# Kernel tuning notes

Hardware: AMD Instinct MI355X
Metric: run time of the kernel (lower is better)

## Reference

```python
import jax, jax.numpy as jnp
import numpy as np

N, D, C = 8192, 10000, 1000


def setup_inputs() -> dict:
    key = jax.random.key(0)
    k1, k2 = jax.random.split(key)
    # binary {0,1} hypervectors, stored as float32 for efficient GEMM-form Hamming distance
    samples = jax.random.randint(k1, (N, D), 0, 2).astype(jnp.float32)
    classes_hv = jax.random.randint(k2, (C, D), 0, 2).astype(jnp.float32)
    return {"samples": samples, "classes_hv": classes_hv}


def reference(samples, classes_hv):
    # Original: response[i] = sum_d xor(samples[:, d], classes_hv[i, d])  (Hamming distance)
    # For binary a,b: xor(a,b) = a + b - 2*a*b, so the full [N, C] distance matrix is
    # dist = row_sum(samples)[:, None] + row_sum(hv)[None, :] - 2 * samples @ hv.T
    # This replaces the per-class XOR+reduce loop with one GEMM (same math).
    s_sum = jnp.sum(samples, axis=-1)          # [N]
    c_sum = jnp.sum(classes_hv, axis=-1)       # [C]
    cross = jnp.einsum('nd,cd->nc', samples, classes_hv)  # [N, C]
    return s_sum[:, None] + c_sum[None, :] - 2.0 * cross  # [N, C] Hamming distances
```

## Files before the change

### kernel.cpp

```cpp
#include <hip/hip_runtime.h>
#include <stdint.h>

#define N_ROWS 8192
#define C_CLS  1000
#define D_DIM  10000
#define W64P   160
#define W32P   (W64P * 2)
#define BKW    16
#define NCHUNK 20

typedef int v4i  __attribute__((ext_vector_type(4)));
typedef int v16i __attribute__((ext_vector_type(16)));

__global__ __launch_bounds__(256) void pack_kernel(
    const float* __restrict__ samples, const float* __restrict__ classes,
    unsigned long long* __restrict__ pA, unsigned long long* __restrict__ pB,
    uint32_t* __restrict__ rsA, uint32_t* __restrict__ rsB)
{
    int gwave = (blockIdx.x * 256 + threadIdx.x) >> 6;
    int lane  = threadIdx.x & 63;
    if (gwave >= N_ROWS + C_CLS) return;

    const float* src;
    unsigned long long* dst;
    uint32_t* rsw;
    if (gwave < N_ROWS) {
        src = samples + (size_t)gwave * D_DIM;
        dst = pA + (size_t)gwave * W64P;
        rsw = rsA + gwave;
    } else {
        int r = gwave - N_ROWS;
        src = classes + (size_t)r * D_DIM;
        dst = pB + (size_t)r * W64P;
        rsw = rsB + r;
    }

    uint32_t rs = 0;
    #pragma unroll 4
    for (int w = 0; w < 40; ++w) {
        int idx = w * 256 + lane * 4;
        float4 v = make_float4(0.f, 0.f, 0.f, 0.f);
        if (idx < D_DIM) v = *(const float4*)(src + idx);
        unsigned long long m0 = __ballot(v.x > 0.5f);
        unsigned long long m1 = __ballot(v.y > 0.5f);
        unsigned long long m2 = __ballot(v.z > 0.5f);
        unsigned long long m3 = __ballot(v.w > 0.5f);
        rs += (uint32_t)(__popcll(m0) + __popcll(m1) + __popcll(m2) + __popcll(m3));
        if (lane == 0) {
            uint4 p0, p1;
            p0.x = (uint32_t)m0; p0.y = (uint32_t)(m0 >> 32);
            p0.z = (uint32_t)m1; p0.w = (uint32_t)(m1 >> 32);
            p1.x = (uint32_t)m2; p1.y = (uint32_t)(m2 >> 32);
            p1.z = (uint32_t)m3; p1.w = (uint32_t)(m3 >> 32);
            *(uint4*)(dst + (size_t)w * 4)     = p0;
            *(uint4*)(dst + (size_t)w * 4 + 2) = p1;
        }
    }
    if (lane == 0) *rsw = rs;
}

__global__ __launch_bounds__(256) void hd_kernel(
    const uint32_t* __restrict__ pA, const uint32_t* __restrict__ pB,
    const uint32_t* __restrict__ rsA, const uint32_t* __restrict__ rsB,
    float* __restrict__ out)
{
    __shared__ uint32_t AsT[2][(BKW / 2) * 256];
    __shared__ uint32_t BsT[2][(BKW / 2) * 256];

    const int tid  = threadIdx.x;
    const int row0 = blockIdx.x * 128;
    const int col0 = blockIdx.y * 128;

    const int w    = tid >> 6;
    const int lane = tid & 63;
    const int wy   = w >> 1;
    const int wx   = w & 1;
    const int ln   = lane & 31;
    const int h4   = (lane >> 5) * 4;
    const int pb   = 2 * w;

    const int srow = tid >> 1;
    const int sq2  = (tid & 1) * 2;
    const uint32_t* gAs = pA + (size_t)(row0 + srow) * W32P + sq2 * 4;
    int gc = col0 + srow; if (gc >= C_CLS) gc = C_CLS - 1;
    const uint32_t* gBs = pB + (size_t)gc * W32P + sq2 * 4;

    uint4 av[2], bv[2];

#define LOADR(ch) do {                                             \
    av[0] = *(const uint4*)(gAs + (ch) * BKW);                     \
    av[1] = *(const uint4*)(gAs + (ch) * BKW + 4);                 \
    bv[0] = *(const uint4*)(gBs + (ch) * BKW);                     \
    bv[1] = *(const uint4*)(gBs + (ch) * BKW + 4);                 \
} while (0)

#define WRITELDS(buf) do {                                         \
    uint32_t* ap_ = &AsT[buf][sq2 * 512 + srow * 2];               \
    *(uint2*)(ap_      ) = make_uint2(av[0].x, av[0].y);           \
    *(uint2*)(ap_ + 256) = make_uint2(av[0].z, av[0].w);           \
    *(uint2*)(ap_ + 512) = make_uint2(av[1].x, av[1].y);           \
    *(uint2*)(ap_ + 768) = make_uint2(av[1].z, av[1].w);           \
    uint32_t* bp_ = &BsT[buf][sq2 * 512 + srow * 2];               \
    *(uint2*)(bp_      ) = make_uint2(bv[0].x, bv[0].y);           \
    *(uint2*)(bp_ + 256) = make_uint2(bv[0].z, bv[0].w);           \
    *(uint2*)(bp_ + 512) = make_uint2(bv[1].x, bv[1].y);           \
    *(uint2*)(bp_ + 768) = make_uint2(bv[1].z, bv[1].w);           \
} while (0)

#define UNP(dst, src) do {                                         \
    dst[0] = (int)(((src) >> (h4 + 0)) & 0x01010101u);             \
    dst[1] = (int)(((src) >> (h4 + 1)) & 0x01010101u);             \
    dst[2] = (int)(((src) >> (h4 + 2)) & 0x01010101u);             \
    dst[3] = (int)(((src) >> (h4 + 3)) & 0x01010101u);             \
} while (0)

#define STEP(wa0_, wa1_, wb0_, wb1_) do {                          \
    v4i a0_, a1_, b0_, b1_;                                        \
    UNP(a0_, wa0_); UNP(b0_, wb0_);                                \
    acc00 = __builtin_amdgcn_mfma_i32_32x32x32_i8(a0_, b0_, acc00, 0, 0, 0); \
    UNP(b1_, wb1_);                                                \
    acc01 = __builtin_amdgcn_mfma_i32_32x32x32_i8(a0_, b1_, acc01, 0, 0, 0); \
    UNP(a1_, wa1_);                                                \
    acc10 = __builtin_amdgcn_mfma_i32_32x32x32_i8(a1_, b0_, acc10, 0, 0, 0); \
    acc11 = __builtin_amdgcn_mfma_i32_32x32x32_i8(a1_, b1_, acc11, 0, 0, 0); \
} while (0)

#define LOADP(set, p) do {                                         \
    ra0[set] = *(const uint2*)&Ac[(p) * 256 + (wy * 64 + ln) * 2];        \
    ra1[set] = *(const uint2*)&Ac[(p) * 256 + (wy * 64 + 32 + ln) * 2];   \
    rb0[set] = *(const uint2*)&Bc[(p) * 256 + (wx * 64 + ln) * 2];        \
    rb1[set] = *(const uint2*)&Bc[(p) * 256 + (wx * 64 + 32 + ln) * 2];   \
} while (0)

    v16i acc00 = {}, acc01 = {}, acc10 = {}, acc11 = {};

    LOADR(0);
    WRITELDS(0);
    __syncthreads();

    #pragma unroll 2
    for (int ch = 0; ch < NCHUNK; ++ch) {
        const int cur = ch & 1;
        if (ch + 1 < NCHUNK) LOADR(ch + 1);

        const uint32_t* Ac = &AsT[cur][0];
        const uint32_t* Bc = &BsT[cur][0];

        uint2 ra0[2], ra1[2], rb0[2], rb1[2];
        LOADP(0, pb & 7);

        #pragma unroll
        for (int i = 0; i < 8; ++i) {
            const int c = i & 1, n = c ^ 1;
            if (i < 7) LOADP(n, (pb + i + 1) & 7);
            __builtin_amdgcn_s_setprio(1);
            STEP(ra0[c].x, ra1[c].x, rb0[c].x, rb1[c].x);
            STEP(ra0[c].y, ra1[c].y, rb0[c].y, rb1[c].y);
            __builtin_amdgcn_s_setprio(0);
        }

        if (ch + 1 < NCHUNK) {
            WRITELDS((ch + 1) & 1);
            __syncthreads();
        }
    }
#undef LOADR
#undef WRITELDS
#undef UNP
#undef STEP
#undef LOADP

    const int gcol0 = col0 + wx * 64 + ln;
    const int gcol1 = gcol0 + 32;
    const uint32_t rb0v = (gcol0 < C_CLS) ? rsB[gcol0] : 0u;
    const uint32_t rb1v = (gcol1 < C_CLS) ? rsB[gcol1] : 0u;
    #pragma unroll
    for (int r = 0; r < 16; ++r) {
        const int m    = (r & 3) + 8 * (r >> 2) + h4;
        const int rowa = row0 + wy * 64 + m;
        const int rowb = rowa + 32;
        const uint32_t ra0v = rsA[rowa];
        const uint32_t ra1v = rsA[rowb];
        if (gcol0 < C_CLS) {
            out[(size_t)rowa * C_CLS + gcol0] =
                (float)(int)(ra0v + rb0v - 2u * (uint32_t)acc00[r]);
            out[(size_t)rowb * C_CLS + gcol0] =
                (float)(int)(ra1v + rb0v - 2u * (uint32_t)acc10[r]);
        }
        if (gcol1 < C_CLS) {
            out[(size_t)rowa * C_CLS + gcol1] =
                (float)(int)(ra0v + rb1v - 2u * (uint32_t)acc01[r]);
            out[(size_t)rowb * C_CLS + gcol1] =
                (float)(int)(ra1v + rb1v - 2u * (uint32_t)acc11[r]);
        }
    }
}

extern "C" void kernel_launch(void* const* d_in, const int* in_sizes, int n_in,
                              void* d_out, int out_size, void* d_ws, size_t ws_size,
                              hipStream_t stream) {
    const float* samples = (const float*)d_in[0];
    const float* classes = (const float*)d_in[1];
    float* out = (float*)d_out;

    unsigned long long* pA = (unsigned long long*)d_ws;
    unsigned long long* pB = pA + (size_t)N_ROWS * W64P;
    uint32_t* rsA = (uint32_t*)(pB + (size_t)C_CLS * W64P);
    uint32_t* rsB = rsA + N_ROWS;

    int waves  = N_ROWS + C_CLS;
    int blocks = (waves + 3) / 4;
    pack_kernel<<<blocks, 256, 0, stream>>>(samples, classes, pA, pB, rsA, rsB);

    dim3 grid(N_ROWS / 128, 8);
    hd_kernel<<<grid, 256, 0, stream>>>((const uint32_t*)pA, (const uint32_t*)pB,
                                        rsA, rsB, out);
}
```

Measured before the change: 543.6 us.

## Stage packed bit tiles via direct global-to-LDS loads with XOR-swizzled layout

Replaces the register-staged global loads and transposed LDS writes with global_load_lds direct copies into a row-major, XOR-swizzled shared layout. Each wave then reads 16-byte vectors per row group instead of 8-byte pairs. This removes the VGPR round-trip and LDS write instructions from the pipeline. The setprio hints and fine-grained LDS prefetch are dropped, which may expose LDS latency before the MFMAs. The loop now syncs every chunk, including the last.

```diff
diff --git a/kernel.cpp b/kernel.cpp
--- a/kernel.cpp
+++ b/kernel.cpp
@@ -64,8 +64,8 @@
     const uint32_t* __restrict__ rsA, const uint32_t* __restrict__ rsB,
     float* __restrict__ out)
 {
-    __shared__ uint32_t AsT[2][(BKW / 2) * 256];
-    __shared__ uint32_t BsT[2][(BKW / 2) * 256];
+    __shared__ uint32_t As[2][128 * BKW];
+    __shared__ uint32_t Bs[2][128 * BKW];
 
     const int tid  = threadIdx.x;
     const int row0 = blockIdx.x * 128;
@@ -77,34 +77,35 @@
     const int wx   = w & 1;
     const int ln   = lane & 31;
     const int h4   = (lane >> 5) * 4;
-    const int pb   = 2 * w;
-
-    const int srow = tid >> 1;
-    const int sq2  = (tid & 1) * 2;
-    const uint32_t* gAs = pA + (size_t)(row0 + srow) * W32P + sq2 * 4;
-    int gc = col0 + srow; if (gc >= C_CLS) gc = C_CLS - 1;
-    const uint32_t* gBs = pB + (size_t)gc * W32P + sq2 * 4;
-
-    uint4 av[2], bv[2];
-
-#define LOADR(ch) do {                                             \
-    av[0] = *(const uint4*)(gAs + (ch) * BKW);                     \
-    av[1] = *(const uint4*)(gAs + (ch) * BKW + 4);                 \
-    bv[0] = *(const uint4*)(gBs + (ch) * BKW);                     \
-    bv[1] = *(const uint4*)(gBs + (ch) * BKW + 4);                 \
-} while (0)
-
-#define WRITELDS(buf) do {                                         \
-    uint32_t* ap_ = &AsT[buf][sq2 * 512 + srow * 2];               \
-    *(uint2*)(ap_      ) = make_uint2(av[0].x, av[0].y);           \
-    *(uint2*)(ap_ + 256) = make_uint2(av[0].z, av[0].w);           \
-    *(uint2*)(ap_ + 512) = make_uint2(av[1].x, av[1].y);           \
-    *(uint2*)(ap_ + 768) = make_uint2(av[1].z, av[1].w);           \
-    uint32_t* bp_ = &BsT[buf][sq2 * 512 + srow * 2];               \
-    *(uint2*)(bp_      ) = make_uint2(bv[0].x, bv[0].y);           \
-    *(uint2*)(bp_ + 256) = make_uint2(bv[0].z, bv[0].w);           \
-    *(uint2*)(bp_ + 512) = make_uint2(bv[1].x, bv[1].y);           \
-    *(uint2*)(bp_ + 768) = make_uint2(bv[1].z, bv[1].w);           \
+    const int sw   = (ln >> 3) & 3;
+
+    const int jrow = lane >> 2;
+    const int jg   = lane & 3;
+    const uint32_t* gA[2];
+    const uint32_t* gB[2];
+    #pragma unroll
+    for (int i = 0; i < 2; ++i) {
+        int r   = (2 * w + i) * 16 + jrow;
+        int key = (r >> 3) & 3;
+        int g   = jg ^ key;
+        gA[i] = pA + (size_t)(row0 + r) * W32P + g * 4;
+        int c = col0 + r;
+        if (c >= C_CLS) c = C_CLS - 1;
+        gB[i] = pB + (size_t)c * W32P + g * 4;
+    }
+
+#define STAGE(ch, buf) do {                                                    \
+    _Pragma("unroll")                                                          \
+    for (int i = 0; i < 2; ++i) {                                              \
+        __builtin_amdgcn_global_load_lds(                                      \
+            (const __attribute__((address_space(1))) uint32_t*)(gA[i] + (ch) * BKW), \
+            (__attribute__((address_space(3))) uint32_t*)&As[buf][(2 * w + i) * 256],\
+            16, 0, 0);                                                         \
+        __builtin_amdgcn_global_load_lds(                                      \
+            (const __attribute__((address_space(1))) uint32_t*)(gB[i] + (ch) * BKW), \
+            (__attribute__((address_space(3))) uint32_t*)&Bs[buf][(2 * w + i) * 256],\
+            16, 0, 0);                                                         \
+    }                                                                          \
 } while (0)
 
 #define UNP(dst, src) do {                                         \
@@ -125,50 +126,40 @@
     acc11 = __builtin_amdgcn_mfma_i32_32x32x32_i8(a1_, b1_, acc11, 0, 0, 0); \
 } while (0)
 
-#define LOADP(set, p) do {                                         \
-    ra0[set] = *(const uint2*)&Ac[(p) * 256 + (wy * 64 + ln) * 2];        \
-    ra1[set] = *(const uint2*)&Ac[(p) * 256 + (wy * 64 + 32 + ln) * 2];   \
-    rb0[set] = *(const uint2*)&Bc[(p) * 256 + (wx * 64 + ln) * 2];        \
-    rb1[set] = *(const uint2*)&Bc[(p) * 256 + (wx * 64 + 32 + ln) * 2];   \
-} while (0)
-
     v16i acc00 = {}, acc01 = {}, acc10 = {}, acc11 = {};
 
-    LOADR(0);
-    WRITELDS(0);
+    const int aoff = (wy * 64 + ln) * BKW;
+    const int boff = (wx * 64 + ln) * BKW;
+
+    STAGE(0, 0);
     __syncthreads();
 
     #pragma unroll 2
     for (int ch = 0; ch < NCHUNK; ++ch) {
         const int cur = ch & 1;
-        if (ch + 1 < NCHUNK) LOADR(ch + 1);
-
-        const uint32_t* Ac = &AsT[cur][0];
-        const uint32_t* Bc = &BsT[cur][0];
-
-        uint2 ra0[2], ra1[2], rb0[2], rb1[2];
-        LOADP(0, pb & 7);
+        if (ch + 1 < NCHUNK) STAGE(ch + 1, cur ^ 1);
+
+        const uint32_t* Ac = &As[cur][0];
+        const uint32_t* Bc = &Bs[cur][0];
 
         #pragma unroll
-        for (int i = 0; i < 8; ++i) {
-            const int c = i & 1, n = c ^ 1;
-            if (i < 7) LOADP(n, (pb + i + 1) & 7);
-            __builtin_amdgcn_s_setprio(1);
-            STEP(ra0[c].x, ra1[c].x, rb0[c].x, rb1[c].x);
-            STEP(ra0[c].y, ra1[c].y, rb0[c].y, rb1[c].y);
-            __builtin_amdgcn_s_setprio(0);
-        }
-
-        if (ch + 1 < NCHUNK) {
-            WRITELDS((ch + 1) & 1);
-            __syncthreads();
-        }
-    }
-#undef LOADR
-#undef WRITELDS
+        for (int g = 0; g < 4; ++g) {
+            const int so = (g ^ sw) << 2;
+            uint4 a0 = *(const uint4*)&Ac[aoff + so];
+            uint4 a1 = *(const uint4*)&Ac[aoff + 512 + so];
+            uint4 b0 = *(const uint4*)&Bc[boff + so];
+            uint4 b1 = *(const uint4*)&Bc[boff + 512 + so];
+            STEP(a0.x, a1.x, b0.x, b1.x);
+            STEP(a0.y, a1.y, b0.y, b1.y);
+            STEP(a0.z, a1.z, b0.z, b1.z);
+            STEP(a0.w, a1.w, b0.w, b1.w);
+        }
+
+        __syncthreads();
+    }
+#undef STAGE
 #undef UNP
 #undef STEP
-#undef LOADP
 
     const int gcol0 = col0 + wx * 64 + ln;
     const int gcol1 = gcol0 + 32;
```

Result: no change. 545.3 us (+0.3%).
